# Kernel tuning notes

Measured on AMD Instinct MI355X. Metric: run time of the kernel, lower is better.

Reference implementation:

```python
import jax, jax.numpy as jnp
import numpy as np
import math

H, E, HD = 12, 768, 64   # heads, embed_dim, per-head hidden
B, S, L = 8, 512, 512    # batch, dec len, enc len
EPS = 1e-12


def layer_norm(x, w, b):
    u = jnp.mean(x, axis=-1, keepdims=True)
    s = jnp.mean((x - u) ** 2, axis=-1, keepdims=True)
    return w * (x - u) / jnp.sqrt(s + EPS) + b


def gelu(x):
    return x * 0.5 * (1.0 + jax.lax.erf(x / math.sqrt(2.0)))


def attention(k, q, w_k, w_q, pw, pb, mask):
    # k:[b,kl,E] q:[b,ql,E] w_k/w_q:[H,E,HD] mask broadcastable to [b,H,ql,kl]
    kx = jnp.einsum('ble,hed->bhld', k, w_k)
    qx = jnp.einsum('bqe,hed->bhqd', q, w_q)
    score = jnp.einsum('bhqd,bhkd->bhqk', qx, kx) / math.sqrt(HD)
    score = jnp.where(mask, score, jnp.asarray(-1e4, score.dtype))
    attn = jax.nn.softmax(score, axis=-1)
    out = jnp.einsum('bhqk,bhkd->bhqd', attn, kx)  # values are kx (as in source)
    b_, h, ql, d = out.shape
    out = out.transpose(0, 2, 1, 3).reshape(b_, ql, h * d)
    return out @ pw + pb


def setup_inputs() -> dict:
    key = jax.random.key(0)
    ks = jax.random.split(key, 16)
    xav = lambda k, shp, fan: jax.random.normal(k, shp, jnp.float32) * math.sqrt(2.0 / fan)
    inp = {
        'X': jax.random.normal(ks[0], (B, S, E), jnp.float32),
        'enc_outputs': jax.random.normal(ks[1], (B, L, E), jnp.float32),
        'enc_valid_lens': jax.random.randint(ks[2], (B,), 1, L + 1, jnp.int32),
        'w_kx1': xav(ks[3], (H, E, HD), E + HD),
        'w_qx1': xav(ks[4], (H, E, HD), E + HD),
        'proj1_w': xav(ks[5], (H * HD, E), 2 * E),
        'proj1_b': jnp.zeros((E,), jnp.float32),
        'ln1_w': jnp.ones((E,), jnp.float32),
        'ln1_b': jnp.zeros((E,), jnp.float32),
        'w_kx2': xav(ks[6], (H, E, HD), E + HD),
        'w_qx2': xav(ks[7], (H, E, HD), E + HD),
        'proj2_w': xav(ks[8], (H * HD, E), 2 * E),
        'proj2_b': jnp.zeros((E,), jnp.float32),
        'ln2_w': jnp.ones((E,), jnp.float32),
        'ln2_b': jnp.zeros((E,), jnp.float32),
        'ffn_w1': xav(ks[9], (E, E), 2 * E),
        'ffn_b1': jnp.zeros((E,), jnp.float32),
        'ffn_w2': xav(ks[10], (E, E), 2 * E),
        'ffn_b2': jnp.zeros((E,), jnp.float32),
        'ln3_w': jnp.ones((E,), jnp.float32),
        'ln3_b': jnp.zeros((E,), jnp.float32),
    }
    return inp


def reference(X, enc_outputs, enc_valid_lens,
              w_kx1, w_qx1, proj1_w, proj1_b, ln1_w, ln1_b,
              w_kx2, w_qx2, proj2_w, proj2_b, ln2_w, ln2_b,
              ffn_w1, ffn_b1, ffn_w2, ffn_b2, ln3_w, ln3_b):
    s = X.shape[1]
    # training path: dec_valid_lens is 2D -> causal mask in Attention
    causal = jnp.tril(jnp.ones((s, s), dtype=bool))[None, None]          # [1,1,s,s]
    X2 = attention(X, X, w_kx1, w_qx1, proj1_w, proj1_b, causal)
    Y = layer_norm(X2 + X, ln1_w, ln1_b)
    # cross mask: key padding from enc_valid_lens (1D branch)
    kl = enc_outputs.shape[1]
    pad = (jnp.arange(kl)[None] < enc_valid_lens[:, None])[:, None, None]  # [b,1,1,kl]
    Y2 = attention(enc_outputs, Y, w_kx2, w_qx2, proj2_w, proj2_b, pad)
    Z = layer_norm(Y2 + Y, ln2_w, ln2_b)
    F = gelu(Z @ ffn_w1 + ffn_b1) @ ffn_w2 + ffn_b2
    return layer_norm(F + Z, ln3_w, ln3_b)
```

## Files before the change

### kernel.cpp

```cpp
#include <hip/hip_runtime.h>
#include <hip/hip_bf16.h>

typedef __hip_bfloat16 bf16;
typedef __attribute__((ext_vector_type(8))) short s8v;
typedef __attribute__((ext_vector_type(4))) short s4v;
typedef __attribute__((ext_vector_type(4))) float f4v;

#define H_ 12
#define E_ 768
#define HD_ 64
#define B_ 8
#define S_ 512
#define M_ 4096

struct P9 { const void* s[8]; bf16* d[8]; const void* vs[10]; bf16* vd[10]; };

typedef __attribute__((address_space(3))) void lds_void;
typedef const __attribute__((address_space(1))) void g_void;

__device__ __forceinline__ void async_copy16(const bf16* g, short* l) {
    __builtin_amdgcn_global_load_lds((g_void*)g, (lds_void*)l, 16, 0, 0);
}

__device__ __forceinline__ float sh2f(short v) {
    unsigned int u = ((unsigned int)(unsigned short)v) << 16;
    return __uint_as_float(u);
}

__device__ __forceinline__ short f2sh(float v) {
    bf16 b = __float2bfloat16(v);
    return *(short*)&b;
}

__device__ __forceinline__ int detect_fp32(const unsigned int* __restrict__ Xh,
                                           int tid, int* scratch) {
    unsigned e = (Xh[tid] >> 7) & 0xFFu;
    int good = (e >= 100u && e <= 141u) ? 1 : 0;
    #pragma unroll
    for (int off = 1; off < 64; off <<= 1) good += __shfl_xor(good, off);
    if ((tid & 63) == 0) scratch[tid >> 6] = good;
    __syncthreads();
    int total = scratch[0] + scratch[1] + scratch[2] + scratch[3];
    return (total <= 154) ? 1 : 0;
}

__device__ __forceinline__ bf16 ldcvt(const void* s, int i, int fp32) {
    return fp32 ? __float2bfloat16(((const float*)s)[i]) : ((const bf16*)s)[i];
}

__global__ __launch_bounds__(256) void prep_kernel(const void* X, const void* enc,
                                                   bf16* Xc, bf16* ENCc,
                                                   P9 p) {
    __shared__ int dsc[4];
    __shared__ float t[64][65];
    const int tid = threadIdx.x;
    const int fp32 = detect_fp32((const unsigned int*)X, tid, dsc);
    const int id = blockIdx.x;

    if (id < 6144) {
        const void* s = (id < 3072) ? X : enc;
        bf16* d = (id < 3072) ? Xc : ENCc;
        int cid = (id < 3072) ? id : id - 3072;
        int i = (cid * 256 + tid) * 4;
        if (fp32) {
            float4 v = *(const float4*)((const float*)s + i);
            bf16 a = __float2bfloat16(v.x), b = __float2bfloat16(v.y),
                 c = __float2bfloat16(v.z), e = __float2bfloat16(v.w);
            s4v o = { *(short*)&a, *(short*)&b, *(short*)&c, *(short*)&e };
            *(s4v*)(d + i) = o;
        } else {
            *(s4v*)(d + i) = *(const s4v*)((const bf16*)s + i);
        }
        return;
    }

    int id2 = id - 6144;
    const int z = id2 / 144;
    const int rem = id2 % 144;
    const int bx = rem % 12, by = rem / 12;

    if (z == 8) {
        int vid = by * 12 + bx;
        if (vid < 10) {
            const void* s = p.vs[vid];
            bf16* d = p.vd[vid];
            for (int i = tid; i < E_; i += 256) d[i] = ldcvt(s, i, fp32);
        }
        return;
    }
    const int c = tid & 63, r0 = tid >> 6;
    if (z < 4) {
        const void* s = p.s[z];
        bf16* d = p.d[z];
        const int e0 = bx * 64, h = by;
        #pragma unroll
        for (int j = 0; j < 16; ++j) {
            int r = r0 * 16 + j;
            int idx = (h * E_ + e0 + r) * HD_ + c;
            t[r][c] = fp32 ? ((const float*)s)[idx] : __bfloat162float(((const bf16*)s)[idx]);
        }
        __syncthreads();
        #pragma unroll
        for (int j = 0; j < 16; ++j) {
            int r = r0 * 16 + j;
            d[(size_t)(h * 64 + r) * E_ + e0 + c] = __float2bfloat16(t[c][r]);
        }
    } else {
        const void* s = p.s[z];
        bf16* d = p.d[z];
        const int k0 = bx * 64, n0 = by * 64;
        #pragma unroll
        for (int j = 0; j < 16; ++j) {
            int r = r0 * 16 + j;
            int idx = (k0 + r) * E_ + n0 + c;
            t[r][c] = fp32 ? ((const float*)s)[idx] : __bfloat162float(((const bf16*)s)[idx]);
        }
        __syncthreads();
        #pragma unroll
        for (int j = 0; j < 16; ++j) {
            int r = r0 * 16 + j;
            d[(size_t)(n0 + r) * E_ + k0 + c] = __float2bfloat16(t[c][r]);
        }
    }
}

template <int EPI>
__global__ __launch_bounds__(256, 4) void gemm3(const bf16* __restrict__ A,
                                                const bf16* __restrict__ Bt,
                                                bf16* __restrict__ C,
                                                const bf16* __restrict__ bias,
                                                const bf16* __restrict__ res) {
    __shared__ short As[64 * 128];
    __shared__ short Bs[64 * 128];
    const int bm = blockIdx.x, bn = blockIdx.y;
    const int tid = threadIdx.x;
    const int w = tid >> 6, l = tid & 63;
    const int wr = (w >> 1) * 32, wc = (w & 1) * 32;
    const int lc = l & 15, quad = l >> 4;
    const int srA = l >> 4, slot = l & 15;

    f4v acc[2][2] = {};

    for (int k0 = 0; k0 < E_; k0 += 128) {
        #pragma unroll
        for (int c = 0; c < 4; ++c) {
            int seg = w * 4 + c;
            int row = seg * 4 + srA;
            int kc = (slot ^ (row & 15)) * 8;
            async_copy16(A + (size_t)(bm * 64 + row) * E_ + k0 + kc, &As[seg * 512]);
            async_copy16(Bt + (size_t)(bn * 64 + row) * E_ + k0 + kc, &Bs[seg * 512]);
        }
        __syncthreads();

        #pragma unroll
        for (int kk = 0; kk < 4; ++kk) {
            s8v a[2], b[2];
            #pragma unroll
            for (int t = 0; t < 2; ++t) {
                int ar = wr + t * 16 + lc;
                a[t] = *(const s8v*)&As[ar * 128 + (((kk * 4 + quad) ^ (ar & 15)) * 8)];
                int bc = wc + t * 16 + lc;
                b[t] = *(const s8v*)&Bs[bc * 128 + (((kk * 4 + quad) ^ (bc & 15)) * 8)];
            }
            acc[0][0] = __builtin_amdgcn_mfma_f32_16x16x32_bf16(a[0], b[0], acc[0][0], 0, 0, 0);
            acc[0][1] = __builtin_amdgcn_mfma_f32_16x16x32_bf16(a[0], b[1], acc[0][1], 0, 0, 0);
            acc[1][0] = __builtin_amdgcn_mfma_f32_16x16x32_bf16(a[1], b[0], acc[1][0], 0, 0, 0);
            acc[1][1] = __builtin_amdgcn_mfma_f32_16x16x32_bf16(a[1], b[1], acc[1][1], 0, 0, 0);
        }
        __syncthreads();
    }

    #pragma unroll
    for (int mt = 0; mt < 2; ++mt)
        #pragma unroll
        for (int nt = 0; nt < 2; ++nt)
            #pragma unroll
            for (int i = 0; i < 4; ++i) {
                int row = bm * 64 + wr + mt * 16 + quad * 4 + i;
                int col = bn * 64 + wc + nt * 16 + lc;
                float v = acc[mt][nt][i];
                if (EPI == 1)
                    v += __bfloat162float(bias[col]) + __bfloat162float(res[(size_t)row * E_ + col]);
                if (EPI == 2) {
                    v += __bfloat162float(bias[col]);
                    v = 0.5f * v * (1.0f + erff(v * 0.70710678118654752f));
                }
                C[(size_t)row * E_ + col] = __float2bfloat16(v);
            }
}

__global__ __launch_bounds__(256, 4) void gemm3q(const bf16* __restrict__ Xc,
                                                 const bf16* __restrict__ ENCc,
                                                 const bf16* __restrict__ Bt,
                                                 bf16* __restrict__ K1,
                                                 bf16* __restrict__ Q1,
                                                 bf16* __restrict__ K2,
                                                 bf16* __restrict__ KT1,
                                                 bf16* __restrict__ KT2) {
    __shared__ short sm[16384];
    const int bm = blockIdx.x, bn = blockIdx.y;
    const int tid = threadIdx.x;
    const int w = tid >> 6, l = tid & 63;
    const int wr = (w >> 1) * 32, wc = (w & 1) * 32;
    const int lc = l & 15, quad = l >> 4;
    const int srA = l >> 3, slot = l & 7;
    const int kc = (slot ^ srA) * 8;

    const bf16* A = (bn >= 24) ? ENCc : Xc;
    const bf16* Ab = A + (size_t)(bm * 64) * E_;
    const bf16* Bb = Bt + (size_t)(bn * 64) * E_;

    f4v acc[2][2] = {};

    #pragma unroll
    for (int c = 0; c < 2; ++c) {
        int seg = w * 2 + c;
        int row = seg * 8 + srA;
        async_copy16(Ab + (size_t)row * E_ + kc, &sm[seg * 512]);
        async_copy16(Bb + (size_t)row * E_ + kc, &sm[8192 + seg * 512]);
    }
    __syncthreads();

    #pragma unroll
    for (int kt = 0; kt < 12; ++kt) {
        const int cur = (kt & 1) * 4096;
        if (kt < 11) {
            const int nxt = ((kt + 1) & 1) * 4096;
            const int k0 = (kt + 1) * 64;
            #pragma unroll
            for (int c = 0; c < 2; ++c) {
                int seg = w * 2 + c;
                int row = seg * 8 + srA;
                async_copy16(Ab + (size_t)row * E_ + k0 + kc, &sm[nxt + seg * 512]);
                async_copy16(Bb + (size_t)row * E_ + k0 + kc, &sm[8192 + nxt + seg * 512]);
            }
        }
        #pragma unroll
        for (int kk = 0; kk < 2; ++kk) {
            s8v a[2], b[2];
            #pragma unroll
            for (int t = 0; t < 2; ++t) {
                int ar = wr + t * 16 + lc;
                a[t] = *(const s8v*)&sm[cur + ar * 64 + (((kk * 4 + quad) ^ (ar & 7)) * 8)];
                int bc = wc + t * 16 + lc;
                b[t] = *(const s8v*)&sm[8192 + cur + bc * 64 + (((kk * 4 + quad) ^ (bc & 7)) * 8)];
            }
            acc[0][0] = __builtin_amdgcn_mfma_f32_16x16x32_bf16(a[0], b[0], acc[0][0], 0, 0, 0);
            acc[0][1] = __builtin_amdgcn_mfma_f32_16x16x32_bf16(a[0], b[1], acc[0][1], 0, 0, 0);
            acc[1][0] = __builtin_amdgcn_mfma_f32_16x16x32_bf16(a[1], b[0], acc[1][0], 0, 0, 0);
            acc[1][1] = __builtin_amdgcn_mfma_f32_16x16x32_bf16(a[1], b[1], acc[1][1], 0, 0, 0);
        }
        __syncthreads();
    }

    const int band = (bn < 12) ? 0 : (bn < 24) ? 1 : 2;
    const int nb = bn - band * 12;
    bf16* C = (band == 0) ? K1 : (band == 1) ? Q1 : K2;

    #pragma unroll
    for (int mt = 0; mt < 2; ++mt)
        #pragma unroll
        for (int nt = 0; nt < 2; ++nt)
            #pragma unroll
            for (int i = 0; i < 4; ++i) {
                int row = bm * 64 + wr + mt * 16 + quad * 4 + i;
                int col = nb * 64 + wc + nt * 16 + lc;
                C[(size_t)row * E_ + col] = __float2bfloat16(acc[mt][nt][i]);
            }

    if (band != 1) {
        bf16* KT = (band == 0) ? KT1 : KT2;
        #pragma unroll
        for (int mt = 0; mt < 2; ++mt)
            #pragma unroll
            for (int nt = 0; nt < 2; ++nt)
                #pragma unroll
                for (int i = 0; i < 4; ++i) {
                    int srow = wr + mt * 16 + quad * 4 + i;
                    int d = wc + nt * 16 + lc;
                    sm[d * 72 + srow] = f2sh(acc[mt][nt][i]);
                }
        __syncthreads();
        const int drow = tid >> 2, c0 = (tid & 3) * 16;
        s8v o0 = *(const s8v*)&sm[drow * 72 + c0];
        s8v o1 = *(const s8v*)&sm[drow * 72 + c0 + 8];
        const int b = bm >> 3, s0 = (bm & 7) * 64;
        bf16* dp = KT + ((size_t)((b * H_ + nb) * 64 + drow) * S_) + s0 + c0;
        *(s8v*)dp = o0;
        *(s8v*)(dp + 8) = o1;
    }
}

template <bool CAUSAL, bool INLQ>
__global__ __launch_bounds__(256) void attn_kernel(const bf16* __restrict__ Q,
                                                   const bf16* __restrict__ Wq,
                                                   const bf16* __restrict__ Kx,
                                                   const bf16* __restrict__ KT,
                                                   bf16* __restrict__ O,
                                                   const int* __restrict__ vlen) {
    __shared__ short qs[64 * 64];
    __shared__ short ks[64 * 64];
    __shared__ short kts[80 * 64];
    __shared__ short ps[64 * 72];

    int bh, qt;
    if (CAUSAL) {
        const signed char Tq[8][3] = {{7,3,0},{7,3,1},{7,4,0},{6,4,1},
                                      {6,4,0},{6,3,1},{5,5,2},{5,2,2}};
        const signed char To[8][3] = {{0,0,0},{1,1,0},{2,0,1},{0,1,1},
                                      {1,2,2},{2,2,2},{0,1,0},{2,1,2}};
        const int id = blockIdx.y * 96 + blockIdx.x;
        const int s = id & 255, j = id >> 8, r = s & 7;
        qt = Tq[r][j];
        bh = (s >> 3) * 3 + To[r][j];
    } else {
        bh = blockIdx.x;
        qt = blockIdx.y;
    }
    const int h = bh % H_, b = bh / H_;
    const int tid = threadIdx.x, w = tid >> 6, l = tid & 63;
    const int lr = (l >> 4) * 4, lc = l & 15, quad = l >> 4;
    const int srA = l >> 3, slot = l & 7;
    const int kc = (slot ^ srA) * 8;
    const int rq = w * 16 + lc;

    {
        int r = 64 + (tid >> 4);
        int c4 = (tid & 15) * 4;
        s4v v = {};
        if (r == 64) { v[0] = 0x3F80; v[1] = 0x3F80; v[2] = 0x3F80; v[3] = 0x3F80; }
        *(s4v*)&kts[r * 64 + c4] = v;
    }

    if (INLQ) {
        const int wr = (w >> 1) * 32, wc = (w & 1) * 32;
        const bf16* Arow = Q + (size_t)(b * S_ + qt * 64) * E_;
        const bf16* Brow = Wq + (size_t)(h * 64) * E_;
        f4v qacc[2][2] = {};
        for (int k0 = 0; k0 < E_; k0 += 64) {
            #pragma unroll
            for (int c = 0; c < 2; ++c) {
                int seg = w * 2 + c;
                int row = seg * 8 + srA;
                async_copy16(Arow + (size_t)row * E_ + k0 + kc, &ks[seg * 512]);
                async_copy16(Brow + (size_t)row * E_ + k0 + kc, &kts[seg * 512]);
            }
            __syncthreads();
            #pragma unroll
            for (int kk = 0; kk < 2; ++kk) {
                s8v a[2], bb[2];
                #pragma unroll
                for (int t = 0; t < 2; ++t) {
                    int ar = wr + t * 16 + lc;
                    a[t] = *(const s8v*)&ks[ar * 64 + (((kk * 4 + quad) ^ (ar & 7)) * 8)];
                    int bc = wc + t * 16 + lc;
                    bb[t] = *(const s8v*)&kts[bc * 64 + (((kk * 4 + quad) ^ (bc & 7)) * 8)];
                }
                qacc[0][0] = __builtin_amdgcn_mfma_f32_16x16x32_bf16(a[0], bb[0], qacc[0][0], 0, 0, 0);
                qacc[0][1] = __builtin_amdgcn_mfma_f32_16x16x32_bf16(a[0], bb[1], qacc[0][1], 0, 0, 0);
                qacc[1][0] = __builtin_amdgcn_mfma_f32_16x16x32_bf16(a[1], bb[0], qacc[1][0], 0, 0, 0);
                qacc[1][1] = __builtin_amdgcn_mfma_f32_16x16x32_bf16(a[1], bb[1], qacc[1][1], 0, 0, 0);
            }
            __syncthreads();
        }
        #pragma unroll
        for (int mt = 0; mt < 2; ++mt)
            #pragma unroll
            for (int nt = 0; nt < 2; ++nt)
                #pragma unroll
                for (int i = 0; i < 4; ++i) {
                    int row = wr + mt * 16 + quad * 4 + i;
                    int d = wc + nt * 16 + lc;
                    qs[row * 64 + (((d >> 3) ^ (row & 7)) * 8) + (d & 7)] = f2sh(qacc[mt][nt][i]);
                }
        __syncthreads();
    } else {
        #pragma unroll
        for (int c = 0; c < 2; ++c) {
            int seg = w * 2 + c;
            int row = seg * 8 + srA;
            async_copy16(Q + ((size_t)(b * S_ + qt * 64 + row) * H_ + h) * HD_ + kc, &qs[seg * 512]);
        }
    }

    const int valid = CAUSAL ? S_ : vlen[b];
    const int kmax = CAUSAL ? (qt + 1) : ((valid + 63) >> 6);

    f4v o_acc[5] = {};
    s8v aq0, aq1;

    for (int kt = 0; kt < kmax; ++kt) {
        #pragma unroll
        for (int c = 0; c < 2; ++c) {
            int seg = w * 2 + c;
            int row = seg * 8 + srA;
            async_copy16(Kx + ((size_t)(b * S_ + kt * 64 + row) * H_ + h) * HD_ + kc, &ks[seg * 512]);
            async_copy16(KT + (size_t)(bh * 64 + row) * S_ + kt * 64 + kc, &kts[seg * 512]);
        }
        __syncthreads();

        if (kt == 0) {
            aq0 = *(const s8v*)&qs[rq * 64 + ((quad ^ (rq & 7)) * 8)];
            aq1 = *(const s8v*)&qs[rq * 64 + (((4 + quad) ^ (rq & 7)) * 8)];
        }

        f4v sacc[4] = {};
        #pragma unroll
        for (int nt = 0; nt < 4; nt++) {
            int rk = nt * 16 + lc;
            s8v bk0 = *(const s8v*)&ks[rk * 64 + ((quad ^ (rk & 7)) * 8)];
            s8v bk1 = *(const s8v*)&ks[rk * 64 + (((4 + quad) ^ (rk & 7)) * 8)];
            sacc[nt] = __builtin_amdgcn_mfma_f32_16x16x32_bf16(aq0, bk0, sacc[nt], 0, 0, 0);
            sacc[nt] = __builtin_amdgcn_mfma_f32_16x16x32_bf16(aq1, bk1, sacc[nt], 0, 0, 0);
        }

        #pragma unroll
        for (int i = 0; i < 4; i++) {
            int qabs = qt * 64 + w * 16 + lr + i;
            #pragma unroll
            for (int nt = 0; nt < 4; nt++) {
                int kabs = kt * 64 + nt * 16 + lc;
                bool ok = CAUSAL ? (kabs <= qabs) : (kabs < valid);
                float sv = ok ? fminf(sacc[nt][i] * 0.125f - 20.0f, 0.0f) : -1.0e4f;
                ps[(w * 16 + lr + i) * 72 + nt * 16 + lc] = f2sh(__expf(sv));
            }
        }

        s8v ap0 = *(const s8v*)&ps[rq * 72 + quad * 8];
        s8v ap1 = *(const s8v*)&ps[rq * 72 + 32 + quad * 8];
        #pragma unroll
        for (int dt = 0; dt < 5; dt++) {
            int rd = dt * 16 + lc;
            s8v bv0 = *(const s8v*)&kts[rd * 64 + ((quad ^ (rd & 7)) * 8)];
            s8v bv1 = *(const s8v*)&kts[rd * 64 + (((4 + quad) ^ (rd & 7)) * 8)];
            o_acc[dt] = __builtin_amdgcn_mfma_f32_16x16x32_bf16(ap0, bv0, o_acc[dt], 0, 0, 0);
            o_acc[dt] = __builtin_amdgcn_mfma_f32_16x16x32_bf16(ap1, bv1, o_acc[dt], 0, 0, 0);
        }
        if (kt + 1 < kmax) __syncthreads();
    }

    float li[4];
    #pragma unroll
    for (int i = 0; i < 4; i++) li[i] = __shfl(o_acc[4][i], (l & 48));

    #pragma unroll
    for (int dt = 0; dt < 4; dt++)
        #pragma unroll
        for (int i = 0; i < 4; i++) {
            int q = qt * 64 + w * 16 + lr + i;
            int d = dt * 16 + lc;
            float v = o_acc[dt][i] / li[i];
            O[((size_t)(b * S_ + q) * H_ + h) * HD_ + d] = __float2bfloat16(v);
        }
}

__global__ __launch_bounds__(256) void ln2_kernel(const bf16* __restrict__ X,
                                                  const bf16* __restrict__ wv,
                                                  const bf16* __restrict__ bv,
                                                  bf16* __restrict__ outb,
                                                  float* __restrict__ outf,
                                                  const unsigned int* __restrict__ Xhead) {
    __shared__ int dsc[4];
    int f32out = 0;
    if (outf != nullptr)
        f32out = detect_fp32(Xhead, threadIdx.x, dsc);
    const int row = blockIdx.x * 4 + (threadIdx.x >> 6);
    const int l = threadIdx.x & 63;
    const bf16* xr = X + (size_t)row * E_;
    s8v v8 = *(const s8v*)(xr + l * 8);
    s4v v4 = *(const s4v*)(xr + 512 + l * 4);
    float x[12];
    #pragma unroll
    for (int j = 0; j < 8; ++j) x[j] = sh2f(v8[j]);
    #pragma unroll
    for (int j = 0; j < 4; ++j) x[8 + j] = sh2f(v4[j]);
    float s = 0.f, ss = 0.f;
    #pragma unroll
    for (int j = 0; j < 12; ++j) { s += x[j]; ss += x[j] * x[j]; }
    #pragma unroll
    for (int off = 1; off < 64; off <<= 1) {
        s += __shfl_xor(s, off);
        ss += __shfl_xor(ss, off);
    }
    float mu = s * (1.0f / E_);
    float var = ss * (1.0f / E_) - mu * mu;
    float rstd = rsqrtf(fmaxf(var, 0.0f) + 1e-12f);
    #pragma unroll
    for (int j = 0; j < 12; ++j) {
        int c = (j < 8) ? (l * 8 + j) : (512 + l * 4 + (j - 8));
        float v = (x[j] - mu) * rstd * __bfloat162float(wv[c]) + __bfloat162float(bv[c]);
        if (f32out) outf[(size_t)row * E_ + c] = v;
        else        outb[(size_t)row * E_ + c] = __float2bfloat16(v);
    }
}

extern "C" void kernel_launch(void* const* d_in, const int* in_sizes, int n_in,
                              void* d_out, int out_size, void* d_ws, size_t ws_size,
                              hipStream_t stream) {
    const void* X = d_in[0];
    const void* enc = d_in[1];
    const int* vlen = (const int*)d_in[2];

    char* ws = (char*)d_ws;
    bf16* vecs = (bf16*)(ws + 256);
    char* wbase = ws + 16384;
    const size_t WSZ = (size_t)E_ * E_ * sizeof(bf16);
    bf16* wk1 = (bf16*)(wbase + 0 * WSZ);
    bf16* wq1 = (bf16*)(wbase + 1 * WSZ);
    bf16* wk2 = (bf16*)(wbase + 2 * WSZ);
    bf16* wq2 = (bf16*)(wbase + 3 * WSZ);
    bf16* p1t = (bf16*)(wbase + 4 * WSZ);
    bf16* p2t = (bf16*)(wbase + 5 * WSZ);
    bf16* f1t = (bf16*)(wbase + 6 * WSZ);
    bf16* f2t = (bf16*)(wbase + 7 * WSZ);
    const size_t ASZ = (size_t)M_ * E_ * sizeof(bf16);
    char* abase = wbase + 8 * WSZ;
    bf16* Xc   = (bf16*)(abase + 0 * ASZ);
    bf16* ENCc = (bf16*)(abase + 1 * ASZ);
    bf16* A0  = (bf16*)(abase + 2 * ASZ);
    bf16* A1  = (bf16*)(abase + 3 * ASZ);
    bf16* A2  = (bf16*)(abase + 4 * ASZ);
    bf16* A3  = (bf16*)(abase + 5 * ASZ);
    bf16* A4  = (bf16*)(abase + 6 * ASZ);
    bf16* A5  = (bf16*)(abase + 7 * ASZ);
    bf16* KT1 = (bf16*)(abase + 8 * ASZ);
    bf16* KT2 = (bf16*)(abase + 9 * ASZ);

    bf16* bias1 = vecs + 0 * E_;
    bf16* lw1   = vecs + 1 * E_;
    bf16* lb1   = vecs + 2 * E_;
    bf16* bias2 = vecs + 3 * E_;
    bf16* lw2   = vecs + 4 * E_;
    bf16* lb2   = vecs + 5 * E_;
    bf16* fb1   = vecs + 6 * E_;
    bf16* fb2   = vecs + 7 * E_;
    bf16* lw3   = vecs + 8 * E_;
    bf16* lb3   = vecs + 9 * E_;

    P9 rp;
    rp.s[0] = d_in[3];  rp.d[0] = wk1;
    rp.s[1] = d_in[4];  rp.d[1] = wq1;
    rp.s[2] = d_in[9];  rp.d[2] = wk2;
    rp.s[3] = d_in[10]; rp.d[3] = wq2;
    rp.s[4] = d_in[5];  rp.d[4] = p1t;
    rp.s[5] = d_in[11]; rp.d[5] = p2t;
    rp.s[6] = d_in[15]; rp.d[6] = f1t;
    rp.s[7] = d_in[17]; rp.d[7] = f2t;
    rp.vs[0] = d_in[6];  rp.vd[0] = bias1;
    rp.vs[1] = d_in[7];  rp.vd[1] = lw1;
    rp.vs[2] = d_in[8];  rp.vd[2] = lb1;
    rp.vs[3] = d_in[12]; rp.vd[3] = bias2;
    rp.vs[4] = d_in[13]; rp.vd[4] = lw2;
    rp.vs[5] = d_in[14]; rp.vd[5] = lb2;
    rp.vs[6] = d_in[16]; rp.vd[6] = fb1;
    rp.vs[7] = d_in[18]; rp.vd[7] = fb2;
    rp.vs[8] = d_in[19]; rp.vd[8] = lw3;
    rp.vs[9] = d_in[20]; rp.vd[9] = lb3;

    prep_kernel<<<7440, 256, 0, stream>>>(X, enc, Xc, ENCc, rp);

    gemm3q<<<dim3(64, 36), 256, 0, stream>>>(Xc, ENCc, wk1, A0, A1, A4, KT1, KT2);

    attn_kernel<true, false><<<dim3(96, 8), 256, 0, stream>>>(A1, nullptr, A0, KT1, A2, nullptr);
    gemm3<1><<<dim3(64, 12), 256, 0, stream>>>(A2, p1t, A3, bias1, Xc);
    ln2_kernel<<<M_ / 4, 256, 0, stream>>>(A3, lw1, lb1, A5, nullptr, nullptr);

    attn_kernel<false, true><<<dim3(96, 8), 256, 0, stream>>>(A5, wq2, A4, KT2, A2, vlen);
    gemm3<1><<<dim3(64, 12), 256, 0, stream>>>(A2, p2t, A3, bias2, A5);
    ln2_kernel<<<M_ / 4, 256, 0, stream>>>(A3, lw2, lb2, A0, nullptr, nullptr);

    gemm3<2><<<dim3(64, 12), 256, 0, stream>>>(A0, f1t, A1, fb1, nullptr);
    gemm3<1><<<dim3(64, 12), 256, 0, stream>>>(A1, f2t, A2, fb2, A0);
    ln2_kernel<<<M_ / 4, 256, 0, stream>>>(A2, lw3, lb3, (bf16*)d_out, (float*)d_out,
                                           (const unsigned int*)X);
}
```

Baseline: 259.3 us.

## Double-buffer gemm3 K-tiles to overlap async global-to-LDS loads with MFMA

The gemm3 kernel now uses a 64-wide K tile held in two LDS buffers. The next tile is prefetched with async global_load_lds while MFMAs run on the current one, replacing the single-buffered 128-wide K loop. The goal is to hide global memory latency behind compute. In exchange it adds more loop iterations, and the swizzle changes to 8 slots per row. The visible diff does not show the trailing sync needed between iterations, so correctness depends on code that is not shown.

```diff
diff --git a/kernel.cpp b/kernel.cpp
--- a/kernel.cpp
+++ b/kernel.cpp
@@ -130,37 +130,52 @@
                                                 bf16* __restrict__ C,
                                                 const bf16* __restrict__ bias,
                                                 const bf16* __restrict__ res) {
-    __shared__ short As[64 * 128];
-    __shared__ short Bs[64 * 128];
+    __shared__ short sm[16384];
     const int bm = blockIdx.x, bn = blockIdx.y;
     const int tid = threadIdx.x;
     const int w = tid >> 6, l = tid & 63;
     const int wr = (w >> 1) * 32, wc = (w & 1) * 32;
     const int lc = l & 15, quad = l >> 4;
-    const int srA = l >> 4, slot = l & 15;
+    const int srA = l >> 3, slot = l & 7;
+    const int kc = (slot ^ srA) * 8;
+
+    const bf16* Ab = A + (size_t)(bm * 64) * E_;
+    const bf16* Bb = Bt + (size_t)(bn * 64) * E_;
 
     f4v acc[2][2] = {};
 
-    for (int k0 = 0; k0 < E_; k0 += 128) {
-        #pragma unroll
-        for (int c = 0; c < 4; ++c) {
-            int seg = w * 4 + c;
-            int row = seg * 4 + srA;
-            int kc = (slot ^ (row & 15)) * 8;
-            async_copy16(A + (size_t)(bm * 64 + row) * E_ + k0 + kc, &As[seg * 512]);
-            async_copy16(Bt + (size_t)(bn * 64 + row) * E_ + k0 + kc, &Bs[seg * 512]);
-        }
-        __syncthreads();
-
-        #pragma unroll
-        for (int kk = 0; kk < 4; ++kk) {
+    #pragma unroll
+    for (int c = 0; c < 2; ++c) {
+        int seg = w * 2 + c;
+        int row = seg * 8 + srA;
+        async_copy16(Ab + (size_t)row * E_ + kc, &sm[seg * 512]);
+        async_copy16(Bb + (size_t)row * E_ + kc, &sm[8192 + seg * 512]);
+    }
+    __syncthreads();
+
+    #pragma unroll
+    for (int kt = 0; kt < 12; ++kt) {
+        const int cur = (kt & 1) * 4096;
+        if (kt < 11) {
+            const int nxt = ((kt + 1) & 1) * 4096;
+            const int k0 = (kt + 1) * 64;
+            #pragma unroll
+            for (int c = 0; c < 2; ++c) {
+                int seg = w * 2 + c;
+                int row = seg * 8 + srA;
+                async_copy16(Ab + (size_t)row * E_ + k0 + kc, &sm[nxt + seg * 512]);
+                async_copy16(Bb + (size_t)row * E_ + k0 + kc, &sm[8192 + nxt + seg * 512]);
+            }
+        }
+        #pragma unroll
+        for (int kk = 0; kk < 2; ++kk) {
             s8v a[2], b[2];
             #pragma unroll
             for (int t = 0; t < 2; ++t) {
                 int ar = wr + t * 16 + lc;
-                a[t] = *(const s8v*)&As[ar * 128 + (((kk * 4 + quad) ^ (ar & 15)) * 8)];
+                a[t] = *(const s8v*)&sm[cur + ar * 64 + (((kk * 4 + quad) ^ (ar & 7)) * 8)];
                 int bc = wc + t * 16 + lc;
-                b[t] = *(const s8v*)&Bs[bc * 128 + (((kk * 4 + quad) ^ (bc & 15)) * 8)];
+                b[t] = *(const s8v*)&sm[8192 + cur + bc * 64 + (((kk * 4 + quad) ^ (bc & 7)) * 8)];
             }
             acc[0][0] = __builtin_amdgcn_mfma_f32_16x16x32_bf16(a[0], b[0], acc[0][0], 0, 0, 0);
             acc[0][1] = __builtin_amdgcn_mfma_f32_16x16x32_bf16(a[0], b[1], acc[0][1], 0, 0, 0);
```

After: 258.0 us, median of 2. No clear change (-0.5%).
